# Performance work log

Measured on AMD Instinct MI355X. Metric: run time of the kernel, lower is better.

Reference implementation:

```python
import jax, jax.numpy as jnp
import numpy as np

N_NODES = 100000


def _gcn_conv(x, W, b, src, dst, num_nodes):
    """PyG-style GCNConv: out = D^{-1/2}(A+I)D^{-1/2} (x W) + b.
    src/dst already include self-loops. Degree over dst with unit edge weights."""
    h = x @ W  # [N, F_out]
    ones = jnp.ones(dst.shape, dtype=h.dtype)
    deg = jax.ops.segment_sum(ones, dst, num_segments=num_nodes)  # [N]
    dinv = jnp.where(deg > 0, jax.lax.rsqrt(deg), 0.0)
    norm = dinv[src] * dinv[dst]  # [E]
    msgs = norm[:, None] * h[src]  # [E, F_out] gather
    agg = jax.ops.segment_sum(msgs, dst, num_segments=num_nodes)  # scatter-add
    return agg + b


def setup_inputs() -> dict:
    key = jax.random.key(0)
    ks = jax.random.split(key, 8)
    N, E = N_NODES, 1600000
    F_in, H, F_out = 128, 128, 64
    x = jax.random.normal(ks[0], (N, F_in), dtype=jnp.float32)
    edge_index = jax.random.randint(ks[1], (2, E), 0, N, dtype=jnp.int32)
    s_in = 1.0 / np.sqrt(F_in)
    s_h = 1.0 / np.sqrt(H)
    s_o = 1.0 / np.sqrt(F_out)
    W1 = jax.random.uniform(ks[2], (F_in, H), jnp.float32, -s_in, s_in)
    b1 = jnp.zeros((H,), jnp.float32)
    W2 = jax.random.uniform(ks[3], (H, F_out), jnp.float32, -s_h, s_h)
    b2 = jnp.zeros((F_out,), jnp.float32)
    Wout = jax.random.uniform(ks[4], (F_out, 1), jnp.float32, -s_o, s_o)
    bout = jax.random.uniform(ks[5], (1,), jnp.float32, -s_o, s_o)
    return {"x": x, "edge_index": edge_index, "W1": W1, "b1": b1,
            "W2": W2, "b2": b2, "Wout": Wout, "bout": bout}


def reference(x, edge_index, W1, b1, W2, b2, Wout, bout):
    N = x.shape[0]
    loops = jnp.arange(N, dtype=edge_index.dtype)
    src = jnp.concatenate([edge_index[0], loops])  # add self-loops
    dst = jnp.concatenate([edge_index[1], loops])
    h = jax.nn.relu(_gcn_conv(x, W1, b1, src, dst, N))
    h = jax.nn.relu(_gcn_conv(h, W2, b2, src, dst, N))
    return h @ Wout + bout  # [N, 1]
```

## Files before the change

kernel.cpp:

```cpp
#include <hip/hip_runtime.h>
#include <math.h>

#define NN 100000
#define CAP 64

typedef _Float16 hv2 __attribute__((ext_vector_type(2)));
typedef _Float16 hv4 __attribute__((ext_vector_type(4)));


__global__ __launch_bounds__(256) void k_fillg(const int* __restrict__ src,
                                               const int* __restrict__ dst,
                                               int* __restrict__ cursor,
                                               int* __restrict__ csr, int E, int NBF,
                                               const float* __restrict__ x,
                                               const float* __restrict__ W,
                                               _Float16* __restrict__ hs, int M) {
    __shared__ float xt[64][132];
    int bid = blockIdx.x;
    int tid = threadIdx.x;
    if (bid & 1) {
        int fid = bid >> 1;
        if (fid >= NBF) return;
        int e0 = fid * 1024 + tid;
        int dd[4], ss[4], pp[4];
        bool ok[4];
        #pragma unroll
        for (int k = 0; k < 4; ++k) {
            int e = e0 + k * 256;
            ok[k] = (e < E);
            dd[k] = ok[k] ? dst[e] : 0;
            ss[k] = ok[k] ? src[e] : 0;
        }
        #pragma unroll
        for (int k = 0; k < 4; ++k)
            if (ok[k]) pp[k] = atomicAdd(&cursor[dd[k]], 1);
        #pragma unroll
        for (int k = 0; k < 4; ++k)
            if (ok[k] && pp[k] < CAP) csr[(size_t)dd[k] * CAP + pp[k]] = ss[k];
        return;
    }
    int gid = bid >> 1;
    int row0 = gid * 64;
    if (row0 >= M) return;
    #pragma unroll
    for (int it = 0; it < 8; ++it) {
        int idx = it * 256 + tid;
        int r = idx >> 5;
        int c4 = (idx & 31) << 2;
        float4 v = make_float4(0.f, 0.f, 0.f, 0.f);
        if (row0 + r < M) v = *(const float4*)&x[(size_t)(row0 + r) * 128 + c4];
        *(float4*)&xt[r][c4] = v;
    }
    __syncthreads();
    int ct = tid & 31, rt = tid >> 5;
    int c0 = ct * 4, r0 = rt * 8;
    float acc[8][4];
    #pragma unroll
    for (int i = 0; i < 8; ++i)
        #pragma unroll
        for (int j = 0; j < 4; ++j) acc[i][j] = 0.f;

    for (int k = 0; k < 128; k += 4) {
        float4 w0 = *(const float4*)&W[(size_t)(k + 0) * 128 + c0];
        float4 w1 = *(const float4*)&W[(size_t)(k + 1) * 128 + c0];
        float4 w2 = *(const float4*)&W[(size_t)(k + 2) * 128 + c0];
        float4 w3 = *(const float4*)&W[(size_t)(k + 3) * 128 + c0];
        #pragma unroll
        for (int i = 0; i < 8; ++i) {
            float4 xv = *(const float4*)&xt[r0 + i][k];
            acc[i][0] += xv.x * w0.x + xv.y * w1.x + xv.z * w2.x + xv.w * w3.x;
            acc[i][1] += xv.x * w0.y + xv.y * w1.y + xv.z * w2.y + xv.w * w3.y;
            acc[i][2] += xv.x * w0.z + xv.y * w1.z + xv.z * w2.z + xv.w * w3.z;
            acc[i][3] += xv.x * w0.w + xv.y * w1.w + xv.z * w2.w + xv.w * w3.w;
        }
    }
    #pragma unroll
    for (int i = 0; i < 8; ++i) {
        int r = row0 + r0 + i;
        if (r < M) {
            hv4 o;
            o.x = (_Float16)acc[i][0];
            o.y = (_Float16)acc[i][1];
            o.z = (_Float16)acc[i][2];
            o.w = (_Float16)acc[i][3];
            *(hv4*)&hs[(size_t)r * 128 + c0] = o;
        }
    }
}


__global__ __launch_bounds__(256) void k_dinvscale(const int* __restrict__ cursor,
                                                   float* __restrict__ dinv,
                                                   _Float16* __restrict__ hs, int n) {
    __shared__ float ds[64];
    int tid = threadIdx.x;
    int row0 = blockIdx.x * 64;
    if (tid < 64) {
        int r = row0 + tid;
        float dv = 0.f;
        if (r < n) {
            dv = rsqrtf((float)(cursor[r] + 1));
            dinv[r] = dv;
        }
        ds[tid] = dv;
    }
    __syncthreads();
    int w = tid >> 6, lane = tid & 63;
    for (int i = w; i < 64; i += 4) {
        int r = row0 + i;
        if (r >= n) break;
        float dv = ds[i];
        hv2* p = (hv2*)&hs[(size_t)r * 128 + 2 * lane];
        hv2 v = *p;
        v.x = (_Float16)((float)v.x * dv);
        v.y = (_Float16)((float)v.y * dv);
        *p = v;
    }
}


__global__ __launch_bounds__(256) void k_agg1(const _Float16* __restrict__ hs,
                                              const int* __restrict__ csr,
                                              const int* __restrict__ cursor,
                                              const float* __restrict__ dinv,
                                              const float* __restrict__ b,
                                              _Float16* __restrict__ out, int n) {
    int wave = (blockIdx.x * 256 + threadIdx.x) >> 6;
    int lane = threadIdx.x & 63;
    if (wave >= n) return;
    int node = wave;
    int start = node * CAP;
    int cnt = __builtin_amdgcn_readfirstlane(cursor[node]);
    cnt = cnt < CAP ? cnt : CAP;
    int h = lane >> 5;
    int f0 = 4 * (lane & 31);

    int my_idx = (lane < cnt) ? csr[start + lane] : 0;

    float a0[4] = {0.f, 0.f, 0.f, 0.f};
    float a1r[4] = {0.f, 0.f, 0.f, 0.f};

    int j = 0;
    for (; j + 16 <= cnt; j += 16) {
        hv4 v[8];
        #pragma unroll
        for (int u = 0; u < 8; ++u) {
            int s = __shfl(my_idx, j + 2 * u + h, 64);
            v[u] = *(const hv4*)(hs + (size_t)s * 128 + f0);
        }
        #pragma unroll
        for (int u = 0; u < 8; ++u) {
            float* a = (u & 1) ? a1r : a0;
            a[0] += (float)v[u].x; a[1] += (float)v[u].y;
            a[2] += (float)v[u].z; a[3] += (float)v[u].w;
        }
    }
    for (; j + 2 <= cnt; j += 2) {
        int s = __shfl(my_idx, j + h, 64);
        hv4 v = *(const hv4*)(hs + (size_t)s * 128 + f0);
        a0[0] += (float)v.x; a0[1] += (float)v.y;
        a0[2] += (float)v.z; a0[3] += (float)v.w;
    }
    if (j < cnt) {
        int s = __shfl(my_idx, j, 64);
        if (h == 0) {
            hv4 v = *(const hv4*)(hs + (size_t)s * 128 + f0);
            a0[0] += (float)v.x; a0[1] += (float)v.y;
            a0[2] += (float)v.z; a0[3] += (float)v.w;
        }
    }
    if (h == 0) {
        hv4 v = *(const hv4*)(hs + (size_t)node * 128 + f0);
        a0[0] += (float)v.x; a0[1] += (float)v.y;
        a0[2] += (float)v.z; a0[3] += (float)v.w;
    }

    float tot[4];
    #pragma unroll
    for (int i = 0; i < 4; ++i) {
        tot[i] = a0[i] + a1r[i];
        tot[i] += __shfl_xor(tot[i], 32, 64);
    }
    float dn = dinv[node];
    float4 bb = *(const float4*)&b[f0];
    hv4 o;
    o.x = (_Float16)fmaxf(dn * tot[0] + bb.x, 0.f);
    o.y = (_Float16)fmaxf(dn * tot[1] + bb.y, 0.f);
    o.z = (_Float16)fmaxf(dn * tot[2] + bb.z, 0.f);
    o.w = (_Float16)fmaxf(dn * tot[3] + bb.w, 0.f);
    if (h == 0)
        __builtin_nontemporal_store(o, (hv4*)&out[(size_t)node * 128 + f0]);
}


__global__ __launch_bounds__(256) void k_gemm2(const _Float16* __restrict__ a,
                                               const float* __restrict__ W,
                                               const float* __restrict__ dinv,
                                               _Float16* __restrict__ hs, int M) {
    __shared__ float xt[64][132];
    int tid = threadIdx.x;
    int row0 = blockIdx.x * 64;
    #pragma unroll
    for (int it = 0; it < 8; ++it) {
        int idx = it * 256 + tid;
        int r = idx >> 5;
        int c4 = (idx & 31) << 2;
        float4 v = make_float4(0.f, 0.f, 0.f, 0.f);
        if (row0 + r < M) {
            hv4 hvv = *(const hv4*)&a[(size_t)(row0 + r) * 128 + c4];
            v = make_float4((float)hvv.x, (float)hvv.y, (float)hvv.z, (float)hvv.w);
        }
        *(float4*)&xt[r][c4] = v;
    }
    __syncthreads();
    int ct = tid & 15, rt = tid >> 4;
    int c0 = ct * 4, r0 = rt * 4;
    float acc[4][4];
    #pragma unroll
    for (int i = 0; i < 4; ++i)
        #pragma unroll
        for (int j = 0; j < 4; ++j) acc[i][j] = 0.f;

    for (int k = 0; k < 128; k += 4) {
        float4 w0 = *(const float4*)&W[(size_t)(k + 0) * 64 + c0];
        float4 w1 = *(const float4*)&W[(size_t)(k + 1) * 64 + c0];
        float4 w2 = *(const float4*)&W[(size_t)(k + 2) * 64 + c0];
        float4 w3 = *(const float4*)&W[(size_t)(k + 3) * 64 + c0];
        #pragma unroll
        for (int i = 0; i < 4; ++i) {
            float4 xv = *(const float4*)&xt[r0 + i][k];
            acc[i][0] += xv.x * w0.x + xv.y * w1.x + xv.z * w2.x + xv.w * w3.x;
            acc[i][1] += xv.x * w0.y + xv.y * w1.y + xv.z * w2.y + xv.w * w3.y;
            acc[i][2] += xv.x * w0.z + xv.y * w1.z + xv.z * w2.z + xv.w * w3.z;
            acc[i][3] += xv.x * w0.w + xv.y * w1.w + xv.z * w2.w + xv.w * w3.w;
        }
    }
    #pragma unroll
    for (int i = 0; i < 4; ++i) {
        int r = row0 + r0 + i;
        if (r < M) {
            float d = dinv[r];
            hv4 o;
            o.x = (_Float16)(acc[i][0] * d);
            o.y = (_Float16)(acc[i][1] * d);
            o.z = (_Float16)(acc[i][2] * d);
            o.w = (_Float16)(acc[i][3] * d);
            *(hv4*)&hs[(size_t)r * 64 + c0] = o;
        }
    }
}


__global__ __launch_bounds__(256) void k_agg2(const _Float16* __restrict__ hs,
                                              const int* __restrict__ csr,
                                              const int* __restrict__ cursor,
                                              const float* __restrict__ dinv,
                                              const float* __restrict__ b2,
                                              const float* __restrict__ Wout,
                                              const float* __restrict__ bout,
                                              float* __restrict__ out, int n) {
    int wave = (blockIdx.x * 256 + threadIdx.x) >> 6;
    int lane = threadIdx.x & 63;
    if (wave >= n) return;
    int node = wave;
    int start = node * CAP;
    int cnt = __builtin_amdgcn_readfirstlane(cursor[node]);
    cnt = cnt < CAP ? cnt : CAP;
    int q = lane >> 4;
    int f0 = 4 * (lane & 15);

    int my_idx = (lane < cnt) ? csr[start + lane] : 0;

    float a0[4] = {0.f, 0.f, 0.f, 0.f};
    float a1r[4] = {0.f, 0.f, 0.f, 0.f};

    int j = 0;
    for (; j + 16 <= cnt; j += 16) {
        hv4 v[4];
        #pragma unroll
        for (int u = 0; u < 4; ++u) {
            int s = __shfl(my_idx, j + 4 * u + q, 64);
            v[u] = *(const hv4*)(hs + (size_t)s * 64 + f0);
        }
        #pragma unroll
        for (int u = 0; u < 4; ++u) {
            float* a = (u & 1) ? a1r : a0;
            a[0] += (float)v[u].x; a[1] += (float)v[u].y;
            a[2] += (float)v[u].z; a[3] += (float)v[u].w;
        }
    }
    for (; j + 4 <= cnt; j += 4) {
        int s = __shfl(my_idx, j + q, 64);
        hv4 v = *(const hv4*)(hs + (size_t)s * 64 + f0);
        a0[0] += (float)v.x; a0[1] += (float)v.y;
        a0[2] += (float)v.z; a0[3] += (float)v.w;
    }
    int rem = cnt - j;
    if (rem > 0) {
        int s = __shfl(my_idx, j + (q < rem ? q : 0), 64);
        if (q < rem) {
            hv4 v = *(const hv4*)(hs + (size_t)s * 64 + f0);
            a0[0] += (float)v.x; a0[1] += (float)v.y;
            a0[2] += (float)v.z; a0[3] += (float)v.w;
        }
    }
    if (q == 0) {
        hv4 v = *(const hv4*)(hs + (size_t)node * 64 + f0);
        a0[0] += (float)v.x; a0[1] += (float)v.y;
        a0[2] += (float)v.z; a0[3] += (float)v.w;
    }

    float tot[4];
    #pragma unroll
    for (int i = 0; i < 4; ++i) {
        tot[i] = a0[i] + a1r[i];
        tot[i] += __shfl_xor(tot[i], 16, 64);
        tot[i] += __shfl_xor(tot[i], 32, 64);
    }
    float dn = dinv[node];
    float4 bb = *(const float4*)&b2[f0];
    float4 wv = *(const float4*)&Wout[f0];
    float p = fmaxf(dn * tot[0] + bb.x, 0.f) * wv.x
            + fmaxf(dn * tot[1] + bb.y, 0.f) * wv.y
            + fmaxf(dn * tot[2] + bb.z, 0.f) * wv.z
            + fmaxf(dn * tot[3] + bb.w, 0.f) * wv.w;
    p += __shfl_xor(p, 1, 64);
    p += __shfl_xor(p, 2, 64);
    p += __shfl_xor(p, 4, 64);
    p += __shfl_xor(p, 8, 64);
    if (lane == 0) __builtin_nontemporal_store(p + bout[0], &out[node]);
}


extern "C" void kernel_launch(void* const* d_in, const int* in_sizes, int n_in,
                              void* d_out, int out_size, void* d_ws, size_t ws_size,
                              hipStream_t stream) {
    const float* x    = (const float*)d_in[0];
    const int*   ei   = (const int*)d_in[1];
    const float* W1   = (const float*)d_in[2];
    const float* b1   = (const float*)d_in[3];
    const float* W2   = (const float*)d_in[4];
    const float* b2   = (const float*)d_in[5];
    const float* Wout = (const float*)d_in[6];
    const float* bout = (const float*)d_in[7];

    const int N = NN;
    const int E = in_sizes[1] / 2;
    const int* src = ei;
    const int* dst = ei + E;

    char* ws = (char*)d_ws;
    size_t off = 0;
    auto alloc = [&](size_t bytes) -> void* {
        void* p = ws + off;
        off = (off + bytes + 255) & ~(size_t)255;
        return p;
    };
    int*      cursor = (int*)alloc((size_t)N * 4);
    float*    dinv   = (float*)alloc((size_t)N * 4);
    int*      csr    = (int*)alloc((size_t)N * CAP * 4);
    _Float16* hs1    = (_Float16*)alloc((size_t)N * 128 * 2);
    _Float16* a1     = (_Float16*)alloc((size_t)N * 128 * 2);
    _Float16* hs2    = hs1;

    (void)hipMemsetAsync(cursor, 0, (size_t)N * 4, stream);

    int NBF = (E + 1023) / 1024;
    int NBG = (N + 63) / 64;
    int NB = NBF > NBG ? NBF : NBG;
    k_fillg<<<2 * NB, 256, 0, stream>>>(src, dst, cursor, csr, E, NBF, x, W1, hs1, N);
    k_dinvscale<<<(N + 63) / 64, 256, 0, stream>>>(cursor, dinv, hs1, N);
    k_agg1 <<<(N + 3) / 4, 256, 0, stream>>>(hs1, csr, cursor, dinv, b1, a1, N);
    k_gemm2<<<(N + 63) / 64, 256, 0, stream>>>(a1, W2, dinv, hs2, N);
    k_agg2 <<<(N + 3) / 4, 256, 0, stream>>>(hs2, csr, cursor, dinv, b2, Wout, bout,
                                             (float*)d_out, N);
}
```

Baseline: 253.3 us.

## Shard per-node edge cursors into eight sub-buckets to spread atomic contention

The CSR fill now keeps eight atomic cursors per destination node, with each block picking a shard from its id and overflowing into the next shard when a 16-slot sub-bucket is full. Degree and the per-node neighbour list are rebuilt by summing the eight shard counts and mapping lanes to sub-bucket slots with wave shuffles. The launch grid also changes from interleaved GEMM and fill blocks to all GEMM blocks first, then all fill blocks. The aim is to cut atomic serialization on hot cursors, at the cost of an 8x larger cursor memset, a doubled CSR buffer, extra atomics on overflow, and more index math in the aggregation kernels.

```diff
diff --git a/kernel.cpp b/kernel.cpp
--- a/kernel.cpp
+++ b/kernel.cpp
@@ -2,7 +2,9 @@
 #include <math.h>
 
 #define NN 100000
-#define CAP 64
+#define NSUB 8
+#define CAPX 16
+#define ROWI 128
 
 typedef _Float16 hv2 __attribute__((ext_vector_type(2)));
 typedef _Float16 hv4 __attribute__((ext_vector_type(4)));
@@ -10,17 +12,18 @@
 
 __global__ __launch_bounds__(256) void k_fillg(const int* __restrict__ src,
                                                const int* __restrict__ dst,
-                                               int* __restrict__ cursor,
-                                               int* __restrict__ csr, int E, int NBF,
+                                               int* __restrict__ cur,
+                                               int* __restrict__ csr, int E,
+                                               int NBG,
                                                const float* __restrict__ x,
                                                const float* __restrict__ W,
                                                _Float16* __restrict__ hs, int M) {
     __shared__ float xt[64][132];
     int bid = blockIdx.x;
     int tid = threadIdx.x;
-    if (bid & 1) {
-        int fid = bid >> 1;
-        if (fid >= NBF) return;
+    if (bid >= NBG) {
+        int fid = bid - NBG;
+        int shard0 = bid & 7;
         int e0 = fid * 1024 + tid;
         int dd[4], ss[4], pp[4];
         bool ok[4];
@@ -33,14 +36,22 @@
         }
         #pragma unroll
         for (int k = 0; k < 4; ++k)
-            if (ok[k]) pp[k] = atomicAdd(&cursor[dd[k]], 1);
-        #pragma unroll
-        for (int k = 0; k < 4; ++k)
-            if (ok[k] && pp[k] < CAP) csr[(size_t)dd[k] * CAP + pp[k]] = ss[k];
+            if (ok[k]) pp[k] = atomicAdd(&cur[shard0 * NN + dd[k]], 1);
+        #pragma unroll
+        for (int k = 0; k < 4; ++k) {
+            if (ok[k]) {
+                int p = pp[k], sub = shard0;
+                #pragma unroll 1
+                for (int t = 0; t < 7 && p >= CAPX; ++t) {
+                    sub = (sub + 1) & 7;
+                    p = atomicAdd(&cur[sub * NN + dd[k]], 1);
+                }
+                if (p < CAPX) csr[(size_t)dd[k] * ROWI + sub * CAPX + p] = ss[k];
+            }
+        }
         return;
     }
-    int gid = bid >> 1;
-    int row0 = gid * 64;
+    int row0 = bid * 64;
     if (row0 >= M) return;
     #pragma unroll
     for (int it = 0; it < 8; ++it) {
@@ -89,7 +100,7 @@
 }
 
 
-__global__ __launch_bounds__(256) void k_dinvscale(const int* __restrict__ cursor,
+__global__ __launch_bounds__(256) void k_dinvscale(const int* __restrict__ cur,
                                                    float* __restrict__ dinv,
                                                    _Float16* __restrict__ hs, int n) {
     __shared__ float ds[64];
@@ -99,7 +110,13 @@
         int r = row0 + tid;
         float dv = 0.f;
         if (r < n) {
-            dv = rsqrtf((float)(cursor[r] + 1));
+            int s = 0;
+            #pragma unroll
+            for (int k = 0; k < NSUB; ++k) {
+                int c = cur[k * NN + r];
+                s += (c < CAPX ? c : CAPX);
+            }
+            dv = rsqrtf((float)(s + 1));
             dinv[r] = dv;
         }
         ds[tid] = dv;
@@ -118,10 +135,29 @@
     }
 }
 
+__device__ __forceinline__ int shard_map(const int* __restrict__ cur, int node,
+                                         int lane, int* sub_out, int* slot_out) {
+    int cc = 0;
+    if (lane < NSUB) {
+        cc = cur[lane * NN + node];
+        cc = cc < CAPX ? cc : CAPX;
+    }
+    int sub = 0, slot = 0, p0 = 0;
+    #pragma unroll
+    for (int k = 0; k < NSUB; ++k) {
+        int ck = __shfl(cc, k, 64);
+        if (lane >= p0 && lane < p0 + ck) { sub = k; slot = lane - p0; }
+        p0 += ck;
+    }
+    *sub_out = sub;
+    *slot_out = slot;
+    return p0 < 64 ? p0 : 64;
+}
+
 
 __global__ __launch_bounds__(256) void k_agg1(const _Float16* __restrict__ hs,
                                               const int* __restrict__ csr,
-                                              const int* __restrict__ cursor,
+                                              const int* __restrict__ cur,
                                               const float* __restrict__ dinv,
                                               const float* __restrict__ b,
                                               _Float16* __restrict__ out, int n) {
@@ -129,13 +165,12 @@
     int lane = threadIdx.x & 63;
     if (wave >= n) return;
     int node = wave;
-    int start = node * CAP;
-    int cnt = __builtin_amdgcn_readfirstlane(cursor[node]);
-    cnt = cnt < CAP ? cnt : CAP;
+    int sub, slot;
+    int cnt = shard_map(cur, node, lane, &sub, &slot);
     int h = lane >> 5;
     int f0 = 4 * (lane & 31);
 
-    int my_idx = (lane < cnt) ? csr[start + lane] : 0;
+    int my_idx = (lane < cnt) ? csr[(size_t)node * ROWI + sub * CAPX + slot] : 0;
 
     float a0[4] = {0.f, 0.f, 0.f, 0.f};
     float a1r[4] = {0.f, 0.f, 0.f, 0.f};
@@ -253,7 +288,7 @@
 
 __global__ __launch_bounds__(256) void k_agg2(const _Float16* __restrict__ hs,
                                               const int* __restrict__ csr,
-                                              const int* __restrict__ cursor,
+                                              const int* __restrict__ cur,
                                               const float* __restrict__ dinv,
                                               const float* __restrict__ b2,
                                               const float* __restrict__ Wout,
@@ -263,13 +298,12 @@
     int lane = threadIdx.x & 63;
     if (wave >= n) return;
     int node = wave;
-    int start = node * CAP;
-    int cnt = __builtin_amdgcn_readfirstlane(cursor[node]);
-    cnt = cnt < CAP ? cnt : CAP;
+    int sub, slot;
+    int cnt = shard_map(cur, node, lane, &sub, &slot);
     int q = lane >> 4;
     int f0 = 4 * (lane & 15);
 
-    int my_idx = (lane < cnt) ? csr[start + lane] : 0;
+    int my_idx = (lane < cnt) ? csr[(size_t)node * ROWI + sub * CAPX + slot] : 0;
 
     float a0[4] = {0.f, 0.f, 0.f, 0.f};
     float a1r[4] = {0.f, 0.f, 0.f, 0.f};
@@ -356,22 +390,21 @@
         off = (off + bytes + 255) & ~(size_t)255;
         return p;
     };
-    int*      cursor = (int*)alloc((size_t)N * 4);
-    float*    dinv   = (float*)alloc((size_t)N * 4);
-    int*      csr    = (int*)alloc((size_t)N * CAP * 4);
-    _Float16* hs1    = (_Float16*)alloc((size_t)N * 128 * 2);
-    _Float16* a1     = (_Float16*)alloc((size_t)N * 128 * 2);
-    _Float16* hs2    = hs1;
-
-    (void)hipMemsetAsync(cursor, 0, (size_t)N * 4, stream);
-
+    int*      cur  = (int*)alloc((size_t)NSUB * N * 4);
+    float*    dinv = (float*)alloc((size_t)N * 4);
+    int*      csr  = (int*)alloc((size_t)N * ROWI * 4);
+    _Float16* hs1  = (_Float16*)alloc((size_t)N * 128 * 2);
+    _Float16* a1   = (_Float16*)alloc((size_t)N * 128 * 2);
+    _Float16* hs2  = hs1;
+
+    (void)hipMemsetAsync(cur, 0, (size_t)NSUB * N * 4, stream);
+
+    int NBG = (N + 63) / 64;
     int NBF = (E + 1023) / 1024;
-    int NBG = (N + 63) / 64;
-    int NB = NBF > NBG ? NBF : NBG;
-    k_fillg<<<2 * NB, 256, 0, stream>>>(src, dst, cursor, csr, E, NBF, x, W1, hs1, N);
-    k_dinvscale<<<(N + 63) / 64, 256, 0, stream>>>(cursor, dinv, hs1, N);
-    k_agg1 <<<(N + 3) / 4, 256, 0, stream>>>(hs1, csr, cursor, dinv, b1, a1, N);
+    k_fillg<<<NBG + NBF, 256, 0, stream>>>(src, dst, cur, csr, E, NBG, x, W1, hs1, N);
+    k_dinvscale<<<(N + 63) / 64, 256, 0, stream>>>(cur, dinv, hs1, N);
+    k_agg1 <<<(N + 3) / 4, 256, 0, stream>>>(hs1, csr, cur, dinv, b1, a1, N);
     k_gemm2<<<(N + 63) / 64, 256, 0, stream>>>(a1, W2, dinv, hs2, N);
-    k_agg2 <<<(N + 3) / 4, 256, 0, stream>>>(hs2, csr, cursor, dinv, b2, Wout, bout,
+    k_agg2 <<<(N + 3) / 4, 256, 0, stream>>>(hs2, csr, cur, dinv, b2, Wout, bout,
                                              (float*)d_out, N);
 }
```

Result: slower. 320.5 us (+26.5%).
